# Performance work log

Hardware: AMD Instinct MI355X
Metric: run time of the kernel (lower is better)

The kernel has to match this reference:

```python
import jax, jax.numpy as jnp
import numpy as np

ALPHA = 8.3  # depth-similarity decay from Depth-aware CNN
K = 3        # kernel size
PAD = 1      # padding (stride=1, dilation=1)


def _patches(x, k, pad):
    """Extract kxk stride-1 patches. x: (B,C,H,W) -> (B,C,k,k,H,W)."""
    B, C, H, W = x.shape
    xp = jnp.pad(x, ((0, 0), (0, 0), (pad, pad), (pad, pad)))
    rows = []
    for i in range(k):
        cols = [xp[:, :, i:i + H, j:j + W] for j in range(k)]
        rows.append(jnp.stack(cols, axis=2))          # (B,C,k,H,W)
    return jnp.stack(rows, axis=2)                     # (B,C,k,k,H,W)


def setup_inputs() -> dict:
    key = jax.random.key(0)
    k1, k2, k3 = jax.random.split(key, 3)
    B, Cin, H, W = 8, 512, 64, 64
    Cout = 64
    x = jax.random.normal(k1, (B, Cin, H, W), dtype=jnp.float32)
    depth = jax.random.uniform(k2, (B, 1, H, W), dtype=jnp.float32)
    stdv = 1.0 / np.sqrt(Cin * K * K)
    weight = jax.random.uniform(k3, (Cout, Cin, K, K), dtype=jnp.float32,
                                minval=-stdv, maxval=stdv)
    return {"input": x, "depth": depth, "weight": weight}


def reference(input, depth, weight):
    # depth-modulated conv: out(p0) = sum_pn w(pn) * x(p0+pn) * exp(-a*|d(p0)-d(p0+pn)|)
    xpat = _patches(input, K, PAD)                 # (B,Cin,K,K,H,W)
    dpat = _patches(depth, K, PAD)                 # (B,1,K,K,H,W)
    d0 = depth[:, :, None, None, :, :]             # center depth (B,1,1,1,H,W)
    gate = jnp.exp(-ALPHA * jnp.abs(d0 - dpat))    # (B,1,K,K,H,W)
    out = jnp.einsum('ocij,bcijhw->bohw', weight, xpat * gate)
    return out
```

## Files before the change

kernel.cpp:

```cpp
#include <hip/hip_runtime.h>
#include <math.h>

#define ALPHA 8.3f
#define STAGE_BYTES 17408

typedef short v8s  __attribute__((ext_vector_type(8)));
typedef float v16f __attribute__((ext_vector_type(16)));
typedef float v4f  __attribute__((ext_vector_type(4)));

static __device__ __forceinline__ unsigned short f2bf(float f) {
    unsigned int u = __float_as_uint(f);
    u = (u + 0x7fffu + ((u >> 16) & 1u)) >> 16;
    return (unsigned short)u;
}

static __device__ __forceinline__ void async16(const void* g, void* l) {
    __builtin_amdgcn_global_load_lds(
        (const __attribute__((address_space(1))) unsigned int*)g,
        (__attribute__((address_space(3))) unsigned int*)l, 16, 0, 0);
}

__global__ void prep_weights(const float* __restrict__ w, unsigned short* __restrict__ wt,
                             float* __restrict__ zb) {
    if (blockIdx.x == 0) zb[threadIdx.x] = 0.f;
    int i = blockIdx.x * 256 + threadIdx.x;
    if (i >= 9 * 32 * 2 * 64 * 8) return;
    int j    = i & 7;
    int lane = (i >> 3) & 63;
    int mt   = (i >> 9) & 1;
    int ks   = (i >> 10) & 31;
    int tap  = i >> 15;
    int o = mt * 32 + (lane & 31);
    int c = ks * 16 + (lane >> 5) * 8 + j;
    wt[i] = f2bf(w[(o * 512 + c) * 9 + tap]);
}

__global__ __launch_bounds__(256) void nhwc_cast(const float* __restrict__ x,
                                                 unsigned short* __restrict__ x2) {
    __shared__ float st[64][65];
    const int bx  = blockIdx.x;
    const int ch2 = bx & 1;
    const int h   = (bx >> 1) & 63;
    const int b   = bx >> 7;
    const int tid = threadIdx.x;
    const float* xb = x + ((size_t)b * 512 + ch2 * 256) * 4096 + h * 64;
    unsigned short* ob = x2 + (((size_t)b * 64 + h) * 64) * 512 + ch2 * 256;
    for (int cb = 0; cb < 4; ++cb) {
        __syncthreads();
#pragma unroll
        for (int i = 0; i < 4; ++i) {
            const int c  = i * 16 + (tid >> 4);
            const int w4 = (tid & 15) * 4;
            const float4 v = *(const float4*)&xb[(size_t)(cb * 64 + c) * 4096 + w4];
            st[c][w4]     = v.x;
            st[c][w4 + 1] = v.y;
            st[c][w4 + 2] = v.z;
            st[c][w4 + 3] = v.w;
        }
        __syncthreads();
#pragma unroll
        for (int j = 0; j < 2; ++j) {
            const int idx = j * 256 + tid;
            const int w = idx >> 3, k = idx & 7;
            unsigned short t[8];
#pragma unroll
            for (int e = 0; e < 8; ++e) t[e] = f2bf(st[k * 8 + e][w]);
            uint4 u;
            u.x = t[0] | ((unsigned)t[1] << 16);
            u.y = t[2] | ((unsigned)t[3] << 16);
            u.z = t[4] | ((unsigned)t[5] << 16);
            u.w = t[6] | ((unsigned)t[7] << 16);
            *(uint4*)&ob[(size_t)w * 512 + cb * 64 + k * 8] = u;
        }
    }
}

__global__ __launch_bounds__(512, 4)
void depthconv_v7(const unsigned short* __restrict__ x2,
                  const float* __restrict__ depth,
                  const unsigned short* __restrict__ wt,
                  const float* __restrict__ zbuf,
                  float* __restrict__ out) {
    __shared__ __align__(16) char smem[2 * STAGE_BYTES];

    const int bx   = blockIdx.x;
    const int xcd  = bx & 7;
    const int i0   = bx >> 3;
    const int wt2  = i0 & 1;
    const int b    = (i0 >> 1) & 7;
    const int ht   = xcd * 4 + (i0 >> 4);
    const int h0 = ht * 2, w0 = wt2 * 32;

    const int tid  = threadIdx.x;
    const int wid  = tid >> 6;
    const int lane = tid & 63;
    const int l31  = lane & 31;
    const int half = lane >> 5;
    const int mt   = wid & 1;
    const int rt   = (wid >> 1) & 1;
    const int kh   = wid >> 2;

    const char* xpix = (const char*)(x2 + ((size_t)b * 4096) * 512);

    float gt[9];
    {
        const float* dp = depth + (size_t)b * 4096;
        const int hq = h0 + rt, wq = w0 + l31;
        const float d0 = dp[hq * 64 + wq];
#pragma unroll
        for (int t = 0; t < 9; ++t) {
            const int hn = hq + t / 3 - 1, wn = wq + t % 3 - 1;
            const float dn = (hn >= 0 && hn < 64 && wn >= 0 && wn < 64) ? dp[hn * 64 + wn] : 0.f;
            gt[t] = __expf(-ALPHA * fabsf(d0 - dn));
        }
    }

    v16f acc;
    v16f vzero;
#pragma unroll
    for (int r = 0; r < 16; ++r) { acc[r] = 0.f; vzero[r] = 0.f; }

#define ISSUE(SS)                                                               \
    {                                                                           \
        const int ss_ = (SS);                                                   \
        char* bufb = smem + (ss_ & 1) * STAGE_BYTES;                            \
        _Pragma("unroll")                                                       \
        for (int it = 0; it < 3; ++it) {                                        \
            const int i = it * 512 + tid;                                       \
            if (i < 1088) {                                                     \
                const int slice = i >> 3;                                       \
                const int gg = (i & 7) ^ (slice & 7);                           \
                const int r = slice / 34;                                       \
                const int c = slice - r * 34;                                   \
                const int hh = h0 - 1 + r, ww = w0 - 1 + c;                     \
                const char* gp = (hh >= 0 && hh < 64 && ww >= 0 && ww < 64)     \
                    ? xpix + (size_t)(hh * 64 + ww) * 1024                      \
                           + (gg >> 2) * 512 + ss_ * 64 + (gg & 3) * 16        \
                    : (const char*)zbuf;                                        \
                async16(gp, bufb + (size_t)i * 16);                             \
            }                                                                   \
        }                                                                       \
    }

    ISSUE(0);

    const int g0 = kh * 4 + half;
    const int g1 = g0 + 2;

    for (int ss = 0; ss < 8; ++ss) {
        __syncthreads();
        if (ss < 7) ISSUE(ss + 1);
        const char* bufb = smem + (ss & 1) * STAGE_BYTES;
        const int ks0 = kh * 16 + ss * 2;
#pragma unroll
        for (int tap = 0; tap < 9; ++tap) {
            const int di = tap / 3, dj = tap % 3;
            const v8s a0 = *(const v8s*)&wt[(((tap * 32 + ks0) * 2 + mt) * 64 + lane) * 8];
            const v8s a1 = *(const v8s*)&wt[(((tap * 32 + ks0 + 1) * 2 + mt) * 64 + lane) * 8];
            const int slice = (rt + di) * 34 + l31 + dj;
            const int s7 = slice & 7;
            const v8s b0 = *(const v8s*)(bufb + ((size_t)(slice * 8 + (g0 ^ s7))) * 16);
            const v8s b1 = *(const v8s*)(bufb + ((size_t)(slice * 8 + (g1 ^ s7))) * 16);
            v16f pass = __builtin_amdgcn_mfma_f32_32x32x16_bf16(a0, b0, vzero, 0, 0, 0);
            pass = __builtin_amdgcn_mfma_f32_32x32x16_bf16(a1, b1, pass, 0, 0, 0);
            const float gv = gt[tap];
#pragma unroll
            for (int r = 0; r < 16; ++r)
                acc[r] = fmaf(gv, pass[r], acc[r]);
        }
    }

    __syncthreads();
    float* red = (float*)smem;
    const int region = mt * 2 + rt;
    if (kh == 1) {
#pragma unroll
        for (int qd = 0; qd < 4; ++qd) {
            v4f v;
            v[0] = acc[qd * 4];     v[1] = acc[qd * 4 + 1];
            v[2] = acc[qd * 4 + 2]; v[3] = acc[qd * 4 + 3];
            *(v4f*)&red[region * 1024 + lane * 16 + qd * 4] = v;
        }
    }
    __syncthreads();
    if (kh == 0) {
        float* ob = out + ((size_t)b * 64) * 4096 + (h0 + rt) * 64 + w0;
#pragma unroll
        for (int qd = 0; qd < 4; ++qd) {
            const v4f v = *(const v4f*)&red[region * 1024 + lane * 16 + qd * 4];
#pragma unroll
            for (int j = 0; j < 4; ++j) {
                const int rg = qd * 4 + j;
                const int o = mt * 32 + (rg & 3) + 8 * (rg >> 2) + 4 * half;
                ob[(size_t)o * 4096 + l31] = acc[rg] + v[j];
            }
        }
    }
}

extern "C" void kernel_launch(void* const* d_in, const int* in_sizes, int n_in,
                              void* d_out, int out_size, void* d_ws, size_t ws_size,
                              hipStream_t stream) {
    const float* x      = (const float*)d_in[0];
    const float* depth  = (const float*)d_in[1];
    const float* weight = (const float*)d_in[2];
    float* out = (float*)d_out;

    unsigned short* wtb = (unsigned short*)d_ws;
    float* zbuf         = (float*)((char*)d_ws + 786432);
    unsigned short* x2  = (unsigned short*)((char*)d_ws + (1 << 20));

    prep_weights<<<1152, 256, 0, stream>>>(weight, wtb, zbuf);
    nhwc_cast<<<1024, 256, 0, stream>>>(x, x2);
    depthconv_v7<<<512, 512, 0, stream>>>(x2, depth, wtb, zbuf, out);
}
```

Before: 141.7 us.

## Reorder weight layout per stage, prefetch weights into registers, split NHWC cast

New measurement: 171.4 us. 20.9% more time.

```diff
diff --git a/kernel.cpp b/kernel.cpp
--- a/kernel.cpp
+++ b/kernel.cpp
@@ -24,12 +24,18 @@
                              float* __restrict__ zb) {
     if (blockIdx.x == 0) zb[threadIdx.x] = 0.f;
     int i = blockIdx.x * 256 + threadIdx.x;
-    if (i >= 9 * 32 * 2 * 64 * 8) return;
+    if (i >= 294912) return;
     int j    = i & 7;
     int lane = (i >> 3) & 63;
-    int mt   = (i >> 9) & 1;
-    int ks   = (i >> 10) & 31;
-    int tap  = i >> 15;
+    int t    = i >> 9;
+    int f    = t % 18;
+    int g    = t / 18;
+    int mt   = g & 1;
+    int kh   = (g >> 1) & 1;
+    int ss   = g >> 2;
+    int tap  = f >> 1;
+    int p    = f & 1;
+    int ks   = kh * 16 + ss * 2 + p;
     int o = mt * 32 + (lane & 31);
     int c = ks * 16 + (lane >> 5) * 8 + j;
     wt[i] = f2bf(w[(o * 512 + c) * 9 + tap]);
@@ -38,45 +44,42 @@
 __global__ __launch_bounds__(256) void nhwc_cast(const float* __restrict__ x,
                                                  unsigned short* __restrict__ x2) {
     __shared__ float st[64][65];
-    const int bx  = blockIdx.x;
-    const int ch2 = bx & 1;
-    const int h   = (bx >> 1) & 63;
-    const int b   = bx >> 7;
+    const int bx = blockIdx.x;
+    const int cq = bx & 7;
+    const int h  = (bx >> 3) & 63;
+    const int b  = bx >> 9;
     const int tid = threadIdx.x;
-    const float* xb = x + ((size_t)b * 512 + ch2 * 256) * 4096 + h * 64;
-    unsigned short* ob = x2 + (((size_t)b * 64 + h) * 64) * 512 + ch2 * 256;
-    for (int cb = 0; cb < 4; ++cb) {
-        __syncthreads();
-#pragma unroll
-        for (int i = 0; i < 4; ++i) {
-            const int c  = i * 16 + (tid >> 4);
-            const int w4 = (tid & 15) * 4;
-            const float4 v = *(const float4*)&xb[(size_t)(cb * 64 + c) * 4096 + w4];
-            st[c][w4]     = v.x;
-            st[c][w4 + 1] = v.y;
-            st[c][w4 + 2] = v.z;
-            st[c][w4 + 3] = v.w;
-        }
-        __syncthreads();
-#pragma unroll
-        for (int j = 0; j < 2; ++j) {
-            const int idx = j * 256 + tid;
-            const int w = idx >> 3, k = idx & 7;
-            unsigned short t[8];
-#pragma unroll
-            for (int e = 0; e < 8; ++e) t[e] = f2bf(st[k * 8 + e][w]);
-            uint4 u;
-            u.x = t[0] | ((unsigned)t[1] << 16);
-            u.y = t[2] | ((unsigned)t[3] << 16);
-            u.z = t[4] | ((unsigned)t[5] << 16);
-            u.w = t[6] | ((unsigned)t[7] << 16);
-            *(uint4*)&ob[(size_t)w * 512 + cb * 64 + k * 8] = u;
-        }
+    const float* xb = x + ((size_t)b * 512 + cq * 64) * 4096 + h * 64;
+    unsigned short* ob = x2 + (((size_t)b * 64 + h) * 64) * 512 + cq * 64;
+#pragma unroll
+    for (int i = 0; i < 4; ++i) {
+        const int c  = i * 16 + (tid >> 4);
+        const int w4 = (tid & 15) * 4;
+        const float4 v = *(const float4*)&xb[(size_t)c * 4096 + w4];
+        st[c][w4]     = v.x;
+        st[c][w4 + 1] = v.y;
+        st[c][w4 + 2] = v.z;
+        st[c][w4 + 3] = v.w;
+    }
+    __syncthreads();
+#pragma unroll
+    for (int j = 0; j < 2; ++j) {
+        const int idx = j * 256 + tid;
+        const int w = idx >> 3, k = idx & 7;
+        unsigned short t[8];
+#pragma unroll
+        for (int e = 0; e < 8; ++e) t[e] = f2bf(st[k * 8 + e][w]);
+        uint4 u;
+        u.x = t[0] | ((unsigned)t[1] << 16);
+        u.y = t[2] | ((unsigned)t[3] << 16);
+        u.z = t[4] | ((unsigned)t[5] << 16);
+        u.w = t[6] | ((unsigned)t[7] << 16);
+        *(uint4*)&ob[(size_t)w * 512 + k * 8] = u;
     }
 }
 
 __global__ __launch_bounds__(512, 4)
-void depthconv_v7(const unsigned short* __restrict__ x2,
+void depthconv_v8(const unsigned short* __restrict__ x2,
                   const float* __restrict__ depth,
                   const unsigned short* __restrict__ wt,
                   const float* __restrict__ zbuf,
@@ -99,26 +102,18 @@
     const int mt   = wid & 1;
     const int rt   = (wid >> 1) & 1;
     const int kh   = wid >> 2;
+    const int wg   = kh * 2 + mt;
 
     const char* xpix = (const char*)(x2 + ((size_t)b * 4096) * 512);
-
-    float gt[9];
-    {
-        const float* dp = depth + (size_t)b * 4096;
-        const int hq = h0 + rt, wq = w0 + l31;
-        const float d0 = dp[hq * 64 + wq];
-#pragma unroll
-        for (int t = 0; t < 9; ++t) {
-            const int hn = hq + t / 3 - 1, wn = wq + t % 3 - 1;
-            const float dn = (hn >= 0 && hn < 64 && wn >= 0 && wn < 64) ? dp[hn * 64 + wn] : 0.f;
-            gt[t] = __expf(-ALPHA * fabsf(d0 - dn));
-        }
-    }
-
-    v16f acc;
-    v16f vzero;
-#pragma unroll
-    for (int r = 0; r < 16; ++r) { acc[r] = 0.f; vzero[r] = 0.f; }
+    const unsigned short* wlane = wt + (size_t)lane * 8;
+
+    v8s A[12];
+#define LOADA(SS)                                                               \
+    {                                                                           \
+        const unsigned short* wp = wlane + (size_t)(((SS) * 4 + wg) * 18) * 512;\
+        _Pragma("unroll")                                                       \
+        for (int f = 0; f < 12; ++f) A[f] = *(const v8s*)(wp + f * 512);        \
+    }
 
 #define ISSUE(SS)                                                               \
     {                                                                           \
@@ -142,7 +137,26 @@
         }                                                                       \
     }
 
+    LOADA(0);
     ISSUE(0);
+
+    float gt[9];
+    {
+        const float* dp = depth + (size_t)b * 4096;
+        const int hq = h0 + rt, wq = w0 + l31;
+        const float d0 = dp[hq * 64 + wq];
+#pragma unroll
+        for (int t = 0; t < 9; ++t) {
+            const int hn = hq + t / 3 - 1, wn = wq + t % 3 - 1;
+            const float dn = (hn >= 0 && hn < 64 && wn >= 0 && wn < 64) ? dp[hn * 64 + wn] : 0.f;
+            gt[t] = __expf(-ALPHA * fabsf(d0 - dn));
+        }
+    }
+
+    v16f acc;
+    v16f vzero;
+#pragma unroll
+    for (int r = 0; r < 16; ++r) { acc[r] = 0.f; vzero[r] = 0.f; }
 
     const int g0 = kh * 4 + half;
     const int g1 = g0 + 2;
@@ -151,12 +165,18 @@
         __syncthreads();
         if (ss < 7) ISSUE(ss + 1);
         const char* bufb = smem + (ss & 1) * STAGE_BYTES;
-        const int ks0 = kh * 16 + ss * 2;
+        const unsigned short* wp = wlane + (size_t)((ss * 4 + wg) * 18) * 512;
 #pragma unroll
         for (int tap = 0; tap < 9; ++tap) {
             const int di = tap / 3, dj = tap % 3;
-            const v8s a0 = *(const v8s*)&wt[(((tap * 32 + ks0) * 2 + mt) * 64 + lane) * 8];
-            const v8s a1 = *(const v8s*)&wt[(((tap * 32 + ks0 + 1) * 2 + mt) * 64 + lane) * 8];
+            v8s a0, a1;
+            if (tap < 6) {
+                a0 = A[tap * 2];
+                a1 = A[tap * 2 + 1];
+            } else {
+                a0 = *(const v8s*)(wp + (tap * 2) * 512);
+                a1 = *(const v8s*)(wp + (tap * 2 + 1) * 512);
+            }
             const int slice = (rt + di) * 34 + l31 + dj;
             const int s7 = slice & 7;
             const v8s b0 = *(const v8s*)(bufb + ((size_t)(slice * 8 + (g0 ^ s7))) * 16);
@@ -168,6 +188,7 @@
             for (int r = 0; r < 16; ++r)
                 acc[r] = fmaf(gv, pass[r], acc[r]);
         }
+        if (ss < 7) LOADA(ss + 1);
     }
 
     __syncthreads();
@@ -211,6 +232,6 @@
     unsigned short* x2  = (unsigned short*)((char*)d_ws + (1 << 20));
 
     prep_weights<<<1152, 256, 0, stream>>>(weight, wtb, zbuf);
-    nhwc_cast<<<1024, 256, 0, stream>>>(x, x2);
-    depthconv_v7<<<512, 512, 0, stream>>>(x2, depth, wtb, zbuf, out);
-}
+    nhwc_cast<<<4096, 256, 0, stream>>>(x, x2);
+    depthconv_v8<<<512, 512, 0, stream>>>(x2, depth, wtb, zbuf, out);
+}
```
